# Performance work log

Measured on AMD Instinct MI355X. Metric: run time of the kernel, lower is better.

Reference implementation:

```python
import jax, jax.numpy as jnp
import numpy as np

B, T, I, H, L = 32768, 30, 4, 64, 32


def _lstm_layer(x, Wih, Whh, bih, bhh):
    """PyTorch-semantics single-layer LSTM, batch_first. Returns (outputs [B,T,H], h_T [B,H])."""
    # Precompute input contribution for all timesteps: [B, T, 4H]
    xg = jnp.einsum('bti,gi->btg', x, Wih) + bih + bhh
    Hh = Whh.shape[1]
    h0 = jnp.zeros((x.shape[0], Hh), x.dtype)

    def step(carry, xg_t):
        h, c = carry
        g = xg_t + h @ Whh.T  # [B, 4H]
        i, f, gg, o = jnp.split(g, 4, axis=-1)  # PyTorch gate order i,f,g,o
        c = jax.nn.sigmoid(f) * c + jax.nn.sigmoid(i) * jnp.tanh(gg)
        h = jax.nn.sigmoid(o) * jnp.tanh(c)
        return (h, c), h

    (hT, _), hs = jax.lax.scan(step, (h0, h0), jnp.swapaxes(xg, 0, 1))
    return jnp.swapaxes(hs, 0, 1), hT


def setup_inputs() -> dict:
    key = jax.random.key(0)
    ks = jax.random.split(key, 20)
    s = 0.1  # weight scale for numerical stability
    inp = {
        'x': jax.random.normal(ks[0], (B, T, I), jnp.float32),
        'enc1_Wih': s * jax.random.normal(ks[1], (4 * H, I), jnp.float32),
        'enc1_Whh': s * jax.random.normal(ks[2], (4 * H, H), jnp.float32),
        'enc1_bih': s * jax.random.normal(ks[3], (4 * H,), jnp.float32),
        'enc1_bhh': s * jax.random.normal(ks[4], (4 * H,), jnp.float32),
        'enc2_Wih': s * jax.random.normal(ks[5], (4 * L, H), jnp.float32),
        'enc2_Whh': s * jax.random.normal(ks[6], (4 * L, L), jnp.float32),
        'enc2_bih': s * jax.random.normal(ks[7], (4 * L,), jnp.float32),
        'enc2_bhh': s * jax.random.normal(ks[8], (4 * L,), jnp.float32),
        'dec1_Wih': s * jax.random.normal(ks[9], (4 * H, L), jnp.float32),
        'dec1_Whh': s * jax.random.normal(ks[10], (4 * H, H), jnp.float32),
        'dec1_bih': s * jax.random.normal(ks[11], (4 * H,), jnp.float32),
        'dec1_bhh': s * jax.random.normal(ks[12], (4 * H,), jnp.float32),
        'dec2_Wih': s * jax.random.normal(ks[13], (4 * I, H), jnp.float32),
        'dec2_Whh': s * jax.random.normal(ks[14], (4 * I, I), jnp.float32),
        'dec2_bih': s * jax.random.normal(ks[15], (4 * I,), jnp.float32),
        'dec2_bhh': s * jax.random.normal(ks[16], (4 * I,), jnp.float32),
    }
    return inp


def reference(x, enc1_Wih, enc1_Whh, enc1_bih, enc1_bhh,
              enc2_Wih, enc2_Whh, enc2_bih, enc2_bhh,
              dec1_Wih, dec1_Whh, dec1_bih, dec1_bhh,
              dec2_Wih, dec2_Whh, dec2_bih, dec2_bhh):
    seq_len = x.shape[1]
    out, _ = _lstm_layer(x, enc1_Wih, enc1_Whh, enc1_bih, enc1_bhh)
    out, h = _lstm_layer(out, enc2_Wih, enc2_Whh, enc2_bih, enc2_bhh)
    latent = jnp.repeat(h[:, None, :], seq_len, axis=1)  # [B, T, L]
    out, _ = _lstm_layer(latent, dec1_Wih, dec1_Whh, dec1_bih, dec1_bhh)
    out, _ = _lstm_layer(out, dec2_Wih, dec2_Whh, dec2_bih, dec2_bhh)
    return out
```

## Files before the change

### kernel.cpp

```cpp
#include <hip/hip_runtime.h>
#include <stdint.h>


typedef unsigned short u16;
typedef unsigned int u32;
typedef __attribute__((ext_vector_type(8))) short bf16x8;
typedef __attribute__((ext_vector_type(4))) float f32x4;
typedef __attribute__((ext_vector_type(4))) u32 u32x4;
typedef __attribute__((ext_vector_type(2))) u32 u32x2;

#define BATCH 32768
#define TT 30
#define IN 4
#define WAVES 8
#define BLOCKT (WAVES * 64)
#define MB 16
#define BPB (WAVES * MB)

#define LOG2E 1.4426950408889634f
#define LOG2E2 2.8853900817779268f

#define O_WHH1 0
#define O_W1C  8192
#define O_WIH2 9216
#define O_WHH2 13312
#define O_WHH3 0
#define O_WIH3 8192
#define O_WIH4 12288
#define O_W4HHF 12800
#define O_B1F 15360
#define O_B2F 15616
#define O_B3F 15744
#define O_B4F 16000
#define O_BUFS 16016
#define PBUF 1088
#define SMEM_WORDS (O_BUFS + WAVES * PBUF)
#define SMEM_BYTES (SMEM_WORDS * 4)

#define WB() __builtin_amdgcn_wave_barrier()
#define MFMA(a, b, c) __builtin_amdgcn_mfma_f32_16x16x32_bf16((a), (b), (c), 0, 0, 0)

__device__ __forceinline__ u16 f2bf(float f) {
    u32 u = __float_as_uint(f);
    u += 0x7fffu + ((u >> 16) & 1u);
    return (u16)(u >> 16);
}
__device__ __forceinline__ float bf2f(u16 v) { return __uint_as_float(((u32)v) << 16); }

__device__ __forceinline__ u32 cvtpk2(float a, float b) {
    u32 d;
    asm("v_cvt_pk_bf16_f32 %0, %1, %2" : "=v"(d) : "v"(a), "v"(b));
    return d;
}

__device__ __forceinline__ float unitH(float yi, float yf, float yg, float yo, float& c) {
    const float ei = __builtin_amdgcn_exp2f(-yi);
    const float ef = __builtin_amdgcn_exp2f(-yf);
    const float eg = __builtin_amdgcn_exp2f(yg);
    const float eo = __builtin_amdgcn_exp2f(-yo);
    const float Z = (1.f + ei) * (1.f + eg);
    const float X = 1.f + ef;
    const float num = fmaf(eg - 1.f, X, c * Z);
    c = num * __builtin_amdgcn_rcpf(X * Z);
    const float ec = __builtin_amdgcn_exp2f(c * LOG2E2);
    return (ec - 1.f) * __builtin_amdgcn_rcpf((1.f + eo) * (1.f + ec));
}

template <int KT, int GS>
__device__ __forceinline__ void stageBh(u16* hi, const float* src, int N, int tid) {
    const int K = KT * 32;
    const int total = N * K;
    for (int idx = tid; idx < total; idx += BLOCKT) {
        const int j = idx & 7;
        const int l = (idx >> 3) & 63;
        const int pr = idx >> 9;
        const int kt = pr & (KT - 1);
        const int nt = pr / KT;
        const int n = (nt << 4) | (l & 15);
        const int k = (kt << 5) + ((l >> 4) << 3) + j;
        const float s = (((n >> GS) & 3) == 2) ? LOG2E2 : LOG2E;
        hi[idx] = f2bf(src[n * K + k] * s);
    }
}

__global__ __launch_bounds__(BLOCKT)
__attribute__((amdgpu_waves_per_eu(2)))
void lstm_ae(
    const float* __restrict__ x,
    const float* __restrict__ w1ih, const float* __restrict__ w1hh,
    const float* __restrict__ b1i, const float* __restrict__ b1h,
    const float* __restrict__ w2ih, const float* __restrict__ w2hh,
    const float* __restrict__ b2i, const float* __restrict__ b2h,
    const float* __restrict__ w3ih, const float* __restrict__ w3hh,
    const float* __restrict__ b3i, const float* __restrict__ b3h,
    const float* __restrict__ w4ih, const float* __restrict__ w4hh,
    const float* __restrict__ b4i, const float* __restrict__ b4h,
    float* __restrict__ out) {
    extern __shared__ float smem[];
    float* W = smem;

    const int tid = threadIdx.x;
    const int wave = tid >> 6, lane = tid & 63;
    const int col = lane & 15, quad = lane >> 4;

    float* pb = smem + O_BUFS + wave * PBUF;
    u16* h1b = (u16*)pb;
    u16* h2b = (u16*)(pb + 512);
    float* gbuf = pb + 768;
    float* bufH4 = pb + 1024;

    const int b0w = blockIdx.x * BPB + wave * MB;
    const int hbase = (col << 3) + ((quad & 1) << 2) + ((quad >> 1) << 7);

    stageBh<2, 6>((u16*)(W + O_WHH1), w1hh, 256, tid);
    stageBh<2, 5>((u16*)(W + O_WIH2), w2ih, 128, tid);
    stageBh<1, 5>((u16*)(W + O_WHH2), w2hh, 128, tid);
    {
        u16* C = (u16*)(W + O_W1C);
        for (int idx = tid; idx < 2048; idx += BLOCKT) {
            const int n = idx >> 3, j = idx & 7;
            const float sc = ((n >> 6) == 2) ? LOG2E2 : LOG2E;
            const float w = w1ih[n * 4 + (j & 3)] * sc;
            C[idx] = (j < 4) ? f2bf(w) : f2bf(w - bf2f(f2bf(w)));
        }
    }
    float* b1f = W + O_B1F;
    float* b2f = W + O_B2F;
    float* b3f = W + O_B3F;
    float* b4f = W + O_B4F;
    for (int i = tid; i < 256; i += BLOCKT)
        b1f[i] = (b1i[i] + b1h[i]) * (((i >> 6) == 2) ? LOG2E2 : LOG2E);
    for (int i = tid; i < 128; i += BLOCKT)
        b2f[i] = (b2i[i] + b2h[i]) * (((i >> 5) == 2) ? LOG2E2 : LOG2E);
    for (int i = tid; i < 256; i += BLOCKT)
        b3f[i] = (b3i[i] + b3h[i]) * (((i >> 6) == 2) ? LOG2E2 : LOG2E);
    for (int i = tid; i < 16; i += BLOCKT)
        b4f[i] = (b4i[i] + b4h[i]) * (((i >> 2) == 2) ? LOG2E2 : LOG2E);
    {
        u32* z = (u32*)pb;
        for (int i = lane; i < 768; i += 64) z[i] = 0u;
    }
    __syncthreads();

    const u16* Whh1hi = (const u16*)(W + O_WHH1);
    const u16* Wih2hi = (const u16*)(W + O_WIH2);
    const u16* Whh2hi = (const u16*)(W + O_WHH2);
    const u16* W1cL = (const u16*)(W + O_W1C) + (col << 3) + ((quad == 1) ? 4 : 0);

    float c1[4][4];
    float c2[2][4];
#pragma unroll
    for (int q = 0; q < 4; ++q)
#pragma unroll
        for (int r = 0; r < 4; ++r) c1[q][r] = 0.f;
#pragma unroll
    for (int q = 0; q < 2; ++q)
#pragma unroll
        for (int r = 0; r < 4; ++r) c2[q][r] = 0.f;

    float4 xcur = *reinterpret_cast<const float4*>(x + ((size_t)(b0w + col) * TT + 0) * IN);

    for (int s = 0; s < TT; ++s) {
        const u32 hi01 = cvtpk2(xcur.x, xcur.y);
        const u32 hi23 = cvtpk2(xcur.z, xcur.w);
        const float r0 = xcur.x - __uint_as_float(hi01 << 16);
        const float r1 = xcur.y - __uint_as_float(hi01 & 0xffff0000u);
        const float r2 = xcur.z - __uint_as_float(hi23 << 16);
        const float r3 = xcur.w - __uint_as_float(hi23 & 0xffff0000u);
        const u32 lo01 = cvtpk2(r0, r1);
        const u32 lo23 = cvtpk2(r2, r3);
        u32x4 xv;
        xv.x = (quad <= 1) ? hi01 : 0u;
        xv.y = (quad <= 1) ? hi23 : 0u;
        xv.z = (quad == 0) ? lo01 : 0u;
        xv.w = (quad == 0) ? lo23 : 0u;
        const bf16x8 a1x = __builtin_bit_cast(bf16x8, xv);
        {
            const int tn = (s + 1 < TT) ? s + 1 : s;
            xcur = *reinterpret_cast<const float4*>(x + ((size_t)(b0w + col) * TT + tn) * IN);
        }
        const bf16x8 a1h0 = *reinterpret_cast<const bf16x8*>(h1b + lane * 8);
        const bf16x8 a1h1 = *reinterpret_cast<const bf16x8*>(h1b + (64 + lane) * 8);
#pragma unroll
        for (int q = 0; q < 4; ++q) {
            f32x4 acc[4];
#pragma unroll
            for (int i = 0; i < 4; ++i) {
                const int nt = i * 4 + q;
                const u32x2 wp = *reinterpret_cast<const u32x2*>(W1cL + nt * 128);
                u32x4 afu;
                afu.x = wp.x; afu.y = wp.y; afu.z = wp.x; afu.w = wp.y;
                const bf16x8 af = __builtin_bit_cast(bf16x8, afu);
                const bf16x8 bh0 = *reinterpret_cast<const bf16x8*>(Whh1hi + ((nt * 2 + 0) * 64 + lane) * 8);
                const bf16x8 bh1 = *reinterpret_cast<const bf16x8*>(Whh1hi + ((nt * 2 + 1) * 64 + lane) * 8);
                f32x4 a = *reinterpret_cast<const f32x4*>(b1f + nt * 16 + (quad << 2));
                a = MFMA(af, a1x, a);
                a = MFMA(bh0, a1h0, a);
                a = MFMA(bh1, a1h1, a);
                acc[i] = a;
            }
            const float h0 = unitH(acc[0][0], acc[1][0], acc[2][0], acc[3][0], c1[q][0]);
            const float h1 = unitH(acc[0][1], acc[1][1], acc[2][1], acc[3][1], c1[q][1]);
            const float h2 = unitH(acc[0][2], acc[1][2], acc[2][2], acc[3][2], c1[q][2]);
            const float h3 = unitH(acc[0][3], acc[1][3], acc[2][3], acc[3][3], c1[q][3]);
            u32x2 wv;
            wv.x = cvtpk2(h0, h1);
            wv.y = cvtpk2(h2, h3);
            *reinterpret_cast<u32x2*>(h1b + hbase + ((q >> 1) << 9) + ((q & 1) << 8)) = wv;
        }
        WB();
        const bf16x8 e1h0 = *reinterpret_cast<const bf16x8*>(h1b + lane * 8);
        const bf16x8 e1h1 = *reinterpret_cast<const bf16x8*>(h1b + (64 + lane) * 8);
        const bf16x8 a2h = *reinterpret_cast<const bf16x8*>(h2b + lane * 8);
        f32x4 acc2[8];
#pragma unroll
        for (int nt = 0; nt < 8; ++nt) {
            const bf16x8 bh0 = *reinterpret_cast<const bf16x8*>(Wih2hi + ((nt * 2 + 0) * 64 + lane) * 8);
            const bf16x8 bh1 = *reinterpret_cast<const bf16x8*>(Wih2hi + ((nt * 2 + 1) * 64 + lane) * 8);
            const bf16x8 ch = *reinterpret_cast<const bf16x8*>(Whh2hi + (nt * 64 + lane) * 8);
            f32x4 a = *reinterpret_cast<const f32x4*>(b2f + nt * 16 + (quad << 2));
            a = MFMA(bh0, e1h0, a);
            a = MFMA(bh1, e1h1, a);
            a = MFMA(ch, a2h, a);
            acc2[nt] = a;
        }
        WB();
#pragma unroll
        for (int q = 0; q < 2; ++q) {
            const float h0 = unitH(acc2[q][0], acc2[2 + q][0], acc2[4 + q][0], acc2[6 + q][0], c2[q][0]);
            const float h1 = unitH(acc2[q][1], acc2[2 + q][1], acc2[4 + q][1], acc2[6 + q][1], c2[q][1]);
            const float h2 = unitH(acc2[q][2], acc2[2 + q][2], acc2[4 + q][2], acc2[6 + q][2], c2[q][2]);
            const float h3 = unitH(acc2[q][3], acc2[2 + q][3], acc2[4 + q][3], acc2[6 + q][3], c2[q][3]);
            u32x2 wv;
            wv.x = cvtpk2(h0, h1);
            wv.y = cvtpk2(h2, h3);
            *reinterpret_cast<u32x2*>(h2b + hbase + (q << 8)) = wv;
        }
        WB();
    }

    __syncthreads();
    stageBh<2, 6>((u16*)(W + O_WHH3), w3hh, 256, tid);
    stageBh<1, 6>((u16*)(W + O_WIH3), w3ih, 256, tid);
    stageBh<2, 2>((u16*)(W + O_WIH4), w4ih, 16, tid);
    for (int i = tid; i < 64; i += BLOCKT)
        W[O_W4HHF + i] = w4hh[i] * ((((i >> 4) & 3) == 2) ? LOG2E2 : LOG2E);

    const bf16x8 aLh = *reinterpret_cast<const bf16x8*>(h2b + lane * 8);
    {
        u32* z = (u32*)pb;
        for (int i = lane; i < 512; i += 64) z[i] = 0u;
        bufH4[lane] = 0.f;
    }
    float c3[4][4];
#pragma unroll
    for (int q = 0; q < 4; ++q)
#pragma unroll
        for (int r = 0; r < 4; ++r) c3[q][r] = 0.f;
    float c4 = 0.f;
    const f32x4 bias4v = *reinterpret_cast<const f32x4*>(b4f + (quad << 2));
    const int u4 = lane & 3, mb = lane >> 2;
    __syncthreads();

    const u16* Whh3hi = (const u16*)(W + O_WHH3);
    const u16* Wih3hi = (const u16*)(W + O_WIH3);
    const u16* Wih4hi = (const u16*)(W + O_WIH4);
    const float* W4hhF = W + O_W4HHF;

    for (int s = 0; s < TT; ++s) {
        const bf16x8 a3h0 = *reinterpret_cast<const bf16x8*>(h1b + lane * 8);
        const bf16x8 a3h1 = *reinterpret_cast<const bf16x8*>(h1b + (64 + lane) * 8);
#pragma unroll
        for (int q = 0; q < 4; ++q) {
            f32x4 acc[4];
#pragma unroll
            for (int i = 0; i < 4; ++i) {
                const int nt = i * 4 + q;
                const bf16x8 bL = *reinterpret_cast<const bf16x8*>(Wih3hi + (nt * 64 + lane) * 8);
                const bf16x8 bh0 = *reinterpret_cast<const bf16x8*>(Whh3hi + ((nt * 2 + 0) * 64 + lane) * 8);
                const bf16x8 bh1 = *reinterpret_cast<const bf16x8*>(Whh3hi + ((nt * 2 + 1) * 64 + lane) * 8);
                f32x4 a = *reinterpret_cast<const f32x4*>(b3f + nt * 16 + (quad << 2));
                a = MFMA(bL, aLh, a);
                a = MFMA(bh0, a3h0, a);
                a = MFMA(bh1, a3h1, a);
                acc[i] = a;
            }
            const float h0 = unitH(acc[0][0], acc[1][0], acc[2][0], acc[3][0], c3[q][0]);
            const float h1 = unitH(acc[0][1], acc[1][1], acc[2][1], acc[3][1], c3[q][1]);
            const float h2 = unitH(acc[0][2], acc[1][2], acc[2][2], acc[3][2], c3[q][2]);
            const float h3 = unitH(acc[0][3], acc[1][3], acc[2][3], acc[3][3], c3[q][3]);
            u32x2 wv;
            wv.x = cvtpk2(h0, h1);
            wv.y = cvtpk2(h2, h3);
            *reinterpret_cast<u32x2*>(h1b + hbase + ((q >> 1) << 9) + ((q & 1) << 8)) = wv;
        }
        WB();
        const bf16x8 d3h0 = *reinterpret_cast<const bf16x8*>(h1b + lane * 8);
        const bf16x8 d3h1 = *reinterpret_cast<const bf16x8*>(h1b + (64 + lane) * 8);
        f32x4 acc4 = bias4v;
        {
            const float4 hv = *reinterpret_cast<const float4*>(bufH4 + (col << 2));
#pragma unroll
            for (int r = 0; r < 4; ++r) {
                const float4 w4 = *reinterpret_cast<const float4*>(W4hhF + ((quad * 4 + r) << 2));
                float sa = acc4[r];
                sa = fmaf(w4.x, hv.x, sa);
                sa = fmaf(w4.y, hv.y, sa);
                sa = fmaf(w4.z, hv.z, sa);
                sa = fmaf(w4.w, hv.w, sa);
                acc4[r] = sa;
            }
        }
        {
            const bf16x8 bh0 = *reinterpret_cast<const bf16x8*>(Wih4hi + (0 * 64 + lane) * 8);
            const bf16x8 bh1 = *reinterpret_cast<const bf16x8*>(Wih4hi + (1 * 64 + lane) * 8);
            acc4 = MFMA(bh0, d3h0, acc4);
            acc4 = MFMA(bh1, d3h1, acc4);
        }
        WB();
        *reinterpret_cast<f32x4*>(gbuf + (col << 4) + (quad << 2)) = acc4;
        WB();
        {
            const float yi = gbuf[mb * 16 + u4];
            const float yf = gbuf[mb * 16 + 4 + u4];
            const float yg = gbuf[mb * 16 + 8 + u4];
            const float yo = gbuf[mb * 16 + 12 + u4];
            const float h = unitH(yi, yf, yg, yo, c4);
            out[((size_t)(b0w + mb) * TT + s) * IN + u4] = h;
            bufH4[mb * 4 + u4] = h;
        }
        WB();
    }
}

extern "C" void kernel_launch(void* const* d_in, const int* in_sizes, int n_in,
                              void* d_out, int out_size, void* d_ws, size_t ws_size,
                              hipStream_t stream) {
    (void)in_sizes; (void)n_in; (void)d_ws; (void)ws_size; (void)out_size;
    hipFuncSetAttribute(reinterpret_cast<const void*>(lstm_ae),
                        hipFuncAttributeMaxDynamicSharedMemorySize, SMEM_BYTES);
    const float* xi = (const float*)d_in[0];
    const float* w1ih = (const float*)d_in[1];
    const float* w1hh = (const float*)d_in[2];
    const float* b1i = (const float*)d_in[3];
    const float* b1h = (const float*)d_in[4];
    const float* w2ih = (const float*)d_in[5];
    const float* w2hh = (const float*)d_in[6];
    const float* b2i = (const float*)d_in[7];
    const float* b2h = (const float*)d_in[8];
    const float* w3ih = (const float*)d_in[9];
    const float* w3hh = (const float*)d_in[10];
    const float* b3i = (const float*)d_in[11];
    const float* b3h = (const float*)d_in[12];
    const float* w4ih = (const float*)d_in[13];
    const float* w4hh = (const float*)d_in[14];
    const float* b4i = (const float*)d_in[15];
    const float* b4h = (const float*)d_in[16];
    float* out = (float*)d_out;

    lstm_ae<<<dim3(BATCH / BPB), dim3(BLOCKT), SMEM_BYTES, stream>>>(
        xi, w1ih, w1hh, b1i, b1h, w2ih, w2hh, b2i, b2h,
        w3ih, w3hh, b3i, b3h, w4ih, w4hh, b4i, b4h, out);
}
```

Baseline: 311.3 us.

## Split LSTM layers across wave roles in clusters with 32x32 MFMA tiles

Restructures the kernel so each block has 4 clusters of 3 waves working on 32 batch rows. Two waves per cluster compute the first layer's gates while the third runs the next layer one timestep behind, giving a software-pipelined wavefront across layers. The MFMA tiles move from 16x16x32 to 32x32x16, and the layer-1 input bias is folded into the input MFMA operand. This trades per-wave wave barriers for block-wide __syncthreads each step and makes the work imbalanced between roles.

```diff
diff --git a/kernel.cpp b/kernel.cpp
--- a/kernel.cpp
+++ b/kernel.cpp
@@ -6,39 +6,41 @@
 typedef unsigned int u32;
 typedef __attribute__((ext_vector_type(8))) short bf16x8;
 typedef __attribute__((ext_vector_type(4))) float f32x4;
+typedef __attribute__((ext_vector_type(16))) float f32x16;
 typedef __attribute__((ext_vector_type(4))) u32 u32x4;
 typedef __attribute__((ext_vector_type(2))) u32 u32x2;
 
 #define BATCH 32768
 #define TT 30
 #define IN 4
-#define WAVES 8
+#define WAVES 12
 #define BLOCKT (WAVES * 64)
-#define MB 16
-#define BPB (WAVES * MB)
+#define MBC 32
+#define NCL 4
+#define BPB (NCL * MBC)
 
 #define LOG2E 1.4426950408889634f
 #define LOG2E2 2.8853900817779268f
 
 #define O_WHH1 0
-#define O_W1C  8192
-#define O_WIH2 9216
-#define O_WHH2 13312
+#define O_FOLD 8192
+#define O_WIH2 10240
+#define O_WHH2 14336
 #define O_WHH3 0
 #define O_WIH3 8192
 #define O_WIH4 12288
 #define O_W4HHF 12800
-#define O_B1F 15360
-#define O_B2F 15616
-#define O_B3F 15744
-#define O_B4F 16000
-#define O_BUFS 16016
-#define PBUF 1088
-#define SMEM_WORDS (O_BUFS + WAVES * PBUF)
+#define O_B2F 16384
+#define O_B3F 16512
+#define O_B4F 16768
+#define O_BUFS 16784
+#define PBUF 1664
+#define SMEM_WORDS (O_BUFS + NCL * PBUF)
 #define SMEM_BYTES (SMEM_WORDS * 4)
 
 #define WB() __builtin_amdgcn_wave_barrier()
-#define MFMA(a, b, c) __builtin_amdgcn_mfma_f32_16x16x32_bf16((a), (b), (c), 0, 0, 0)
+#define MFMA32(a, b, c) __builtin_amdgcn_mfma_f32_32x32x16_bf16((a), (b), (c), 0, 0, 0)
+#define MFMA16(a, b, c) __builtin_amdgcn_mfma_f32_16x16x32_bf16((a), (b), (c), 0, 0, 0)
 
 __device__ __forceinline__ u16 f2bf(float f) {
     u32 u = __float_as_uint(f);
@@ -66,8 +68,25 @@
     return (ec - 1.f) * __builtin_amdgcn_rcpf((1.f + eo) * (1.f + ec));
 }
 
+template <int KT16, int GS>
+__device__ __forceinline__ void stage32(u16* dst, const float* src, int N, int tid) {
+    const int K = KT16 * 16;
+    const int total = N * K;
+    for (int idx = tid; idx < total; idx += BLOCKT) {
+        const int j = idx & 7;
+        const int l = (idx >> 3) & 63;
+        const int pr = idx >> 9;
+        const int kt = pr % KT16;
+        const int nt = pr / KT16;
+        const int n = nt * 32 + (l & 31);
+        const int k = kt * 16 + ((l >> 5) << 3) + j;
+        const float s = (((n >> GS) & 3) == 2) ? LOG2E2 : LOG2E;
+        dst[idx] = f2bf(src[n * K + k] * s);
+    }
+}
+
 template <int KT, int GS>
-__device__ __forceinline__ void stageBh(u16* hi, const float* src, int N, int tid) {
+__device__ __forceinline__ void stage16(u16* dst, const float* src, int N, int tid) {
     const int K = KT * 32;
     const int total = N * K;
     for (int idx = tid; idx < total; idx += BLOCKT) {
@@ -79,12 +98,97 @@
         const int n = (nt << 4) | (l & 15);
         const int k = (kt << 5) + ((l >> 4) << 3) + j;
         const float s = (((n >> GS) & 3) == 2) ? LOG2E2 : LOG2E;
-        hi[idx] = f2bf(src[n * K + k] * s);
-    }
-}
+        dst[idx] = f2bf(src[n * K + k] * s);
+    }
+}
+
+#define LD8(P, IDX) (*reinterpret_cast<const bf16x8*>((P) + ((IDX) * 64 + lane) * 8))
+
+#define BINIT(DST, BP, RB)                                                               \
+    _Pragma("unroll") for (int p_ = 0; p_ < 4; ++p_) {                                   \
+        const f32x4 b_ = *reinterpret_cast<const f32x4*>((BP) + (RB) + p_ * 8 + 4 * hi); \
+        (DST)[4 * p_ + 0] = b_[0]; (DST)[4 * p_ + 1] = b_[1];                            \
+        (DST)[4 * p_ + 2] = b_[2]; (DST)[4 * p_ + 3] = b_[3];                            \
+    }
+
+#define CELL16(AI, AF, AG, AO, CST, IMG, BKT)                                                        \
+    _Pragma("unroll") for (int p_ = 0; p_ < 4; ++p_) {                                               \
+        const float h0_ = unitH((AI)[4*p_+0], (AF)[4*p_+0], (AG)[4*p_+0], (AO)[4*p_+0], (CST)[4*p_+0]); \
+        const float h1_ = unitH((AI)[4*p_+1], (AF)[4*p_+1], (AG)[4*p_+1], (AO)[4*p_+1], (CST)[4*p_+1]); \
+        const float h2_ = unitH((AI)[4*p_+2], (AF)[4*p_+2], (AG)[4*p_+2], (AO)[4*p_+2], (CST)[4*p_+2]); \
+        const float h3_ = unitH((AI)[4*p_+3], (AF)[4*p_+3], (AG)[4*p_+3], (AO)[4*p_+3], (CST)[4*p_+3]); \
+        u32x2 wv_;                                                                                   \
+        wv_.x = cvtpk2(h0_, h1_);                                                                    \
+        wv_.y = cvtpk2(h2_, h3_);                                                                    \
+        *reinterpret_cast<u32x2*>((IMG) + (((BKT) + (p_ >> 1)) * 64 + (p_ & 1) * 32 + c31) * 8 + 4 * hi) = wv_; \
+    }
+
+#define E1G(DST, G) {                                                  \
+        f32x16 a_ = MFMA32(foldr[G], xB, z16);                         \
+        a_ = MFMA32(LD8(Whh1p, (2 * (G) + role) * 4 + 0), h1B0, a_);   \
+        a_ = MFMA32(LD8(Whh1p, (2 * (G) + role) * 4 + 1), h1B1, a_);   \
+        a_ = MFMA32(LD8(Whh1p, (2 * (G) + role) * 4 + 2), h1B2, a_);   \
+        a_ = MFMA32(LD8(Whh1p, (2 * (G) + role) * 4 + 3), h1B3, a_);   \
+        DST = a_; }
+
+#define E2G(DST, G) {                                                  \
+        f32x16 a_; BINIT(a_, b2f, (G) * 32)                            \
+        a_ = MFMA32(LD8(Wih2p, (G) * 4 + 0), h1B0, a_);                \
+        a_ = MFMA32(LD8(Wih2p, (G) * 4 + 1), h1B1, a_);                \
+        a_ = MFMA32(LD8(Wih2p, (G) * 4 + 2), h1B2, a_);                \
+        a_ = MFMA32(LD8(Wih2p, (G) * 4 + 3), h1B3, a_);                \
+        a_ = MFMA32(LD8(Whh2p, (G) * 2 + 0), h2B0, a_);                \
+        a_ = MFMA32(LD8(Whh2p, (G) * 2 + 1), h2B1, a_);                \
+        DST = a_; }
+
+#define D1G(DST, G) {                                                  \
+        f32x16 a_; BINIT(a_, b3f, (2 * (G) + role) * 32)               \
+        a_ = MFMA32(LD8(Wih3p, (2 * (G) + role) * 2 + 0), latB0, a_);  \
+        a_ = MFMA32(LD8(Wih3p, (2 * (G) + role) * 2 + 1), latB1, a_);  \
+        a_ = MFMA32(LD8(Whh3p, (2 * (G) + role) * 4 + 0), h3B0, a_);   \
+        a_ = MFMA32(LD8(Whh3p, (2 * (G) + role) * 4 + 1), h3B1, a_);   \
+        a_ = MFMA32(LD8(Whh3p, (2 * (G) + role) * 4 + 2), h3B2, a_);   \
+        a_ = MFMA32(LD8(Whh3p, (2 * (G) + role) * 4 + 3), h3B3, a_);   \
+        DST = a_; }
+#define D1G0(DST, G) {                                                 \
+        f32x16 a_; BINIT(a_, b3f, (2 * (G) + role) * 32)               \
+        a_ = MFMA32(LD8(Wih3p, (2 * (G) + role) * 2 + 0), latB0, a_);  \
+        a_ = MFMA32(LD8(Wih3p, (2 * (G) + role) * 2 + 1), latB1, a_);  \
+        DST = a_; }
+
+#define D2ADDR(M, BH) ((((2 * (M) + (quad >> 1)) * 64) + (quad & 1) * 32 + (BH) * 16 + col16) * 8)
+
+#define DEC2BODY(T) {                                                                   \
+        f32x4 a0 = b4v, a1 = b4v;                                                       \
+        _Pragma("unroll") for (int r_ = 0; r_ < 4; ++r_) {                              \
+            float s0 = a0[r_], s1 = a1[r_];                                             \
+            s0 = fmaf(w4r[r_].x, hv0.x, s0); s0 = fmaf(w4r[r_].y, hv0.y, s0);           \
+            s0 = fmaf(w4r[r_].z, hv0.z, s0); s0 = fmaf(w4r[r_].w, hv0.w, s0);           \
+            s1 = fmaf(w4r[r_].x, hv1.x, s1); s1 = fmaf(w4r[r_].y, hv1.y, s1);           \
+            s1 = fmaf(w4r[r_].z, hv1.z, s1); s1 = fmaf(w4r[r_].w, hv1.w, s1);           \
+            a0[r_] = s0; a1[r_] = s1;                                                   \
+        }                                                                               \
+        a0 = MFMA16(w4a0, dB00, a0); a0 = MFMA16(w4a1, dB10, a0);                       \
+        a1 = MFMA16(w4a0, dB01, a1); a1 = MFMA16(w4a1, dB11, a1);                       \
+        WB();                                                                           \
+        *reinterpret_cast<f32x4*>(gbuf + col16 * 16 + quad * 4) = a0;                   \
+        *reinterpret_cast<f32x4*>(gbuf + (16 + col16) * 16 + quad * 4) = a1;            \
+        WB();                                                                           \
+        {                                                                               \
+            const int u4_ = lane & 3, mb_ = lane >> 2;                                  \
+            const float h0_ = unitH(gbuf[mb_ * 16 + u4_], gbuf[mb_ * 16 + 4 + u4_],     \
+                                    gbuf[mb_ * 16 + 8 + u4_], gbuf[mb_ * 16 + 12 + u4_], c4a); \
+            out[((size_t)(b0w + mb_) * TT + (T)) * IN + u4_] = h0_;                     \
+            bufH4[mb_ * 4 + u4_] = h0_;                                                 \
+            const int b1_ = 16 + mb_;                                                   \
+            const float h1_ = unitH(gbuf[b1_ * 16 + u4_], gbuf[b1_ * 16 + 4 + u4_],     \
+                                    gbuf[b1_ * 16 + 8 + u4_], gbuf[b1_ * 16 + 12 + u4_], c4b); \
+            out[((size_t)(b0w + b1_) * TT + (T)) * IN + u4_] = h1_;                     \
+            bufH4[b1_ * 4 + u4_] = h1_;                                                 \
+        }                                                                               \
+        WB(); }
 
 __global__ __launch_bounds__(BLOCKT)
-__attribute__((amdgpu_waves_per_eu(2)))
 void lstm_ae(
     const float* __restrict__ x,
     const float* __restrict__ w1ih, const float* __restrict__ w1hh,
@@ -101,235 +205,223 @@
 
     const int tid = threadIdx.x;
     const int wave = tid >> 6, lane = tid & 63;
-    const int col = lane & 15, quad = lane >> 4;
-
-    float* pb = smem + O_BUFS + wave * PBUF;
-    u16* h1b = (u16*)pb;
-    u16* h2b = (u16*)(pb + 512);
-    float* gbuf = pb + 768;
-    float* bufH4 = pb + 1024;
-
-    const int b0w = blockIdx.x * BPB + wave * MB;
-    const int hbase = (col << 3) + ((quad & 1) << 2) + ((quad >> 1) << 7);
-
-    stageBh<2, 6>((u16*)(W + O_WHH1), w1hh, 256, tid);
-    stageBh<2, 5>((u16*)(W + O_WIH2), w2ih, 128, tid);
-    stageBh<1, 5>((u16*)(W + O_WHH2), w2hh, 128, tid);
+    const int cl = wave / 3, role = wave % 3;
+    const int c31 = lane & 31, hi = lane >> 5;
+    const int col16 = lane & 15, quad = lane >> 4;
+
+    float* pb = smem + O_BUFS + cl * PBUF;
+    u16* h1img = (u16*)pb;
+    u16* h2img = (u16*)(pb + 1024);
+    float* gbuf = pb + 1024;
+    float* bufH4 = pb + 1536;
+
+    const int b0w = blockIdx.x * BPB + cl * MBC;
+
+    stage32<4, 6>((u16*)(W + O_WHH1), w1hh, 256, tid);
+    stage32<4, 5>((u16*)(W + O_WIH2), w2ih, 128, tid);
+    stage32<2, 5>((u16*)(W + O_WHH2), w2hh, 128, tid);
     {
-        u16* C = (u16*)(W + O_W1C);
-        for (int idx = tid; idx < 2048; idx += BLOCKT) {
-            const int n = idx >> 3, j = idx & 7;
-            const float sc = ((n >> 6) == 2) ? LOG2E2 : LOG2E;
-            const float w = w1ih[n * 4 + (j & 3)] * sc;
-            C[idx] = (j < 4) ? f2bf(w) : f2bf(w - bf2f(f2bf(w)));
+        u16* F = (u16*)(W + O_FOLD);
+        for (int idx = tid; idx < 4096; idx += BLOCKT) {
+            const int j = idx & 7;
+            const int l = (idx >> 3) & 63;
+            const int nt = idx >> 9;
+            const int m = nt * 32 + (l & 31);
+            const int hif = l >> 5;
+            const float sc = ((m >> 6) == 2) ? LOG2E2 : LOG2E;
+            u16 v = 0;
+            if (!hif) {
+                v = f2bf(w1ih[m * 4 + (j & 3)] * sc);
+            } else if (j < 4) {
+                const float w = w1ih[m * 4 + j] * sc;
+                v = f2bf(w - bf2f(f2bf(w)));
+            } else if (j == 4) {
+                v = f2bf((b1i[m] + b1h[m]) * sc);
+            } else if (j == 5) {
+                const float b = (b1i[m] + b1h[m]) * sc;
+                v = f2bf(b - bf2f(f2bf(b)));
+            }
+            F[idx] = v;
         }
     }
-    float* b1f = W + O_B1F;
     float* b2f = W + O_B2F;
     float* b3f = W + O_B3F;
     float* b4f = W + O_B4F;
-    for (int i = tid; i < 256; i += BLOCKT)
-        b1f[i] = (b1i[i] + b1h[i]) * (((i >> 6) == 2) ? LOG2E2 : LOG2E);
     for (int i = tid; i < 128; i += BLOCKT)
         b2f[i] = (b2i[i] + b2h[i]) * (((i >> 5) == 2) ? LOG2E2 : LOG2E);
     for (int i = tid; i < 256; i += BLOCKT)
         b3f[i] = (b3i[i] + b3h[i]) * (((i >> 6) == 2) ? LOG2E2 : LOG2E);
     for (int i = tid; i < 16; i += BLOCKT)
         b4f[i] = (b4i[i] + b4h[i]) * (((i >> 2) == 2) ? LOG2E2 : LOG2E);
-    {
-        u32* z = (u32*)pb;
-        for (int i = lane; i < 768; i += 64) z[i] = 0u;
+    if (role == 2) {
+        u32* z = (u32*)h2img;
+        for (int i = lane; i < 512; i += 64) z[i] = 0u;
     }
     __syncthreads();
 
-    const u16* Whh1hi = (const u16*)(W + O_WHH1);
-    const u16* Wih2hi = (const u16*)(W + O_WIH2);
-    const u16* Whh2hi = (const u16*)(W + O_WHH2);
-    const u16* W1cL = (const u16*)(W + O_W1C) + (col << 3) + ((quad == 1) ? 4 : 0);
-
-    float c1[4][4];
-    float c2[2][4];
+    const u16* Whh1p = (const u16*)(W + O_WHH1);
+    const u16* Wih2p = (const u16*)(W + O_WIH2);
+    const u16* Whh2p = (const u16*)(W + O_WHH2);
+    const u16* FOLDp = (const u16*)(W + O_FOLD);
+
+    const f32x16 z16 = {0.f, 0.f, 0.f, 0.f, 0.f, 0.f, 0.f, 0.f,
+                        0.f, 0.f, 0.f, 0.f, 0.f, 0.f, 0.f, 0.f};
+    float cst[16];
 #pragma unroll
-    for (int q = 0; q < 4; ++q)
+    for (int r = 0; r < 16; ++r) cst[r] = 0.f;
+
+    bf16x8 foldr[4] = {};
+    if (role < 2) {
 #pragma unroll
-        for (int r = 0; r < 4; ++r) c1[q][r] = 0.f;
-#pragma unroll
-    for (int q = 0; q < 2; ++q)
-#pragma unroll
-        for (int r = 0; r < 4; ++r) c2[q][r] = 0.f;
-
-    float4 xcur = *reinterpret_cast<const float4*>(x + ((size_t)(b0w + col) * TT + 0) * IN);
-
-    for (int s = 0; s < TT; ++s) {
-        const u32 hi01 = cvtpk2(xcur.x, xcur.y);
-        const u32 hi23 = cvtpk2(xcur.z, xcur.w);
-        const float r0 = xcur.x - __uint_as_float(hi01 << 16);
-        const float r1 = xcur.y - __uint_as_float(hi01 & 0xffff0000u);
-        const float r2 = xcur.z - __uint_as_float(hi23 << 16);
-        const float r3 = xcur.w - __uint_as_float(hi23 & 0xffff0000u);
-        const u32 lo01 = cvtpk2(r0, r1);
-        const u32 lo23 = cvtpk2(r2, r3);
-        u32x4 xv;
-        xv.x = (quad <= 1) ? hi01 : 0u;
-        xv.y = (quad <= 1) ? hi23 : 0u;
-        xv.z = (quad == 0) ? lo01 : 0u;
-        xv.w = (quad == 0) ? lo23 : 0u;
-        const bf16x8 a1x = __builtin_bit_cast(bf16x8, xv);
-        {
-            const int tn = (s + 1 < TT) ? s + 1 : s;
-            xcur = *reinterpret_cast<const float4*>(x + ((size_t)(b0w + col) * TT + tn) * IN);
+        for (int g = 0; g < 4; ++g) foldr[g] = LD8(FOLDp, 2 * g + role);
+    }
+
+    float4 xcur = {0.f, 0.f, 0.f, 0.f};
+    if (role < 2)
+        xcur = *reinterpret_cast<const float4*>(x + ((size_t)(b0w + c31) * TT + 0) * IN);
+
+    auto buildX = [&](const float4 xc) -> bf16x8 {
+        const u32 h01 = cvtpk2(xc.x, xc.y);
+        const u32 h23 = cvtpk2(xc.z, xc.w);
+        const float r0 = xc.x - __uint_as_float(h01 << 16);
+        const float r1 = xc.y - __uint_as_float(h01 & 0xffff0000u);
+        const float r2 = xc.z - __uint_as_float(h23 << 16);
+        const float r3 = xc.w - __uint_as_float(h23 & 0xffff0000u);
+        const u32 l01 = cvtpk2(r0, r1);
+        const u32 l23 = cvtpk2(r2, r3);
+        u32x4 v;
+        v.x = h01;
+        v.y = h23;
+        v.z = hi ? 0x3F803F80u : l01;
+        v.w = hi ? 0u : l23;
+        return __builtin_bit_cast(bf16x8, v);
+    };
+
+    if (role < 2) {
+        const bf16x8 xB = buildX(xcur);
+        xcur = *reinterpret_cast<const float4*>(x + ((size_t)(b0w + c31) * TT + 1) * IN);
+        f32x16 aI = MFMA32(foldr[0], xB, z16);
+        f32x16 aF = MFMA32(foldr[1], xB, z16);
+        f32x16 aG = MFMA32(foldr[2], xB, z16);
+        f32x16 aO = MFMA32(foldr[3], xB, z16);
+        CELL16(aI, aF, aG, aO, cst, h1img, 2 * role)
+    }
+    __syncthreads();
+
+    for (int t = 0; t < TT - 1; ++t) {
+        const bf16x8 h1B0 = *reinterpret_cast<const bf16x8*>(h1img + (0 * 64 + lane) * 8);
+        const bf16x8 h1B1 = *reinterpret_cast<const bf16x8*>(h1img + (1 * 64 + lane) * 8);
+        const bf16x8 h1B2 = *reinterpret_cast<const bf16x8*>(h1img + (2 * 64 + lane) * 8);
+        const bf16x8 h1B3 = *reinterpret_cast<const bf16x8*>(h1img + (3 * 64 + lane) * 8);
+        bf16x8 h2B0 = {}, h2B1 = {};
+        if (role == 2) {
+            h2B0 = *reinterpret_cast<const bf16x8*>(h2img + (0 * 64 + lane) * 8);
+            h2B1 = *reinterpret_cast<const bf16x8*>(h2img + (1 * 64 + lane) * 8);
         }
-        const bf16x8 a1h0 = *reinterpret_cast<const bf16x8*>(h1b + lane * 8);
-        const bf16x8 a1h1 = *reinterpret_cast<const bf16x8*>(h1b + (64 + lane) * 8);
-#pragma unroll
-        for (int q = 0; q < 4; ++q) {
-            f32x4 acc[4];
-#pragma unroll
-            for (int i = 0; i < 4; ++i) {
-                const int nt = i * 4 + q;
-                const u32x2 wp = *reinterpret_cast<const u32x2*>(W1cL + nt * 128);
-                u32x4 afu;
-                afu.x = wp.x; afu.y = wp.y; afu.z = wp.x; afu.w = wp.y;
-                const bf16x8 af = __builtin_bit_cast(bf16x8, afu);
-                const bf16x8 bh0 = *reinterpret_cast<const bf16x8*>(Whh1hi + ((nt * 2 + 0) * 64 + lane) * 8);
-                const bf16x8 bh1 = *reinterpret_cast<const bf16x8*>(Whh1hi + ((nt * 2 + 1) * 64 + lane) * 8);
-                f32x4 a = *reinterpret_cast<const f32x4*>(b1f + nt * 16 + (quad << 2));
-                a = MFMA(af, a1x, a);
-                a = MFMA(bh0, a1h0, a);
-                a = MFMA(bh1, a1h1, a);
-                acc[i] = a;
-            }
-            const float h0 = unitH(acc[0][0], acc[1][0], acc[2][0], acc[3][0], c1[q][0]);
-            const float h1 = unitH(acc[0][1], acc[1][1], acc[2][1], acc[3][1], c1[q][1]);
-            const float h2 = unitH(acc[0][2], acc[1][2], acc[2][2], acc[3][2], c1[q][2]);
-            const float h3 = unitH(acc[0][3], acc[1][3], acc[2][3], acc[3][3], c1[q][3]);
-            u32x2 wv;
-            wv.x = cvtpk2(h0, h1);
-            wv.y = cvtpk2(h2, h3);
-            *reinterpret_cast<u32x2*>(h1b + hbase + ((q >> 1) << 9) + ((q & 1) << 8)) = wv;
+        __syncthreads();
+        if (role == 2) {
+            f32x16 aI, aF, aG, aO;
+            E2G(aI, 0) E2G(aF, 1) E2G(aG, 2) E2G(aO, 3)
+            CELL16(aI, aF, aG, aO, cst, h2img, 0)
+        } else {
+            const bf16x8 xB = buildX(xcur);
+            const int tn = (t + 2 < TT) ? t + 2 : TT - 1;
+            xcur = *reinterpret_cast<const float4*>(x + ((size_t)(b0w + c31) * TT + tn) * IN);
+            f32x16 aI, aF, aG, aO;
+            E1G(aI, 0) E1G(aF, 1) E1G(aG, 2) E1G(aO, 3)
+            CELL16(aI, aF, aG, aO, cst, h1img, 2 * role)
         }
-        WB();
-        const bf16x8 e1h0 = *reinterpret_cast<const bf16x8*>(h1b + lane * 8);
-        const bf16x8 e1h1 = *reinterpret_cast<const bf16x8*>(h1b + (64 + lane) * 8);
-        const bf16x8 a2h = *reinterpret_cast<const bf16x8*>(h2b + lane * 8);
-        f32x4 acc2[8];
-#pragma unroll
-        for (int nt = 0; nt < 8; ++nt) {
-            const bf16x8 bh0 = *reinterpret_cast<const bf16x8*>(Wih2hi + ((nt * 2 + 0) * 64 + lane) * 8);
-            const bf16x8 bh1 = *reinterpret_cast<const bf16x8*>(Wih2hi + ((nt * 2 + 1) * 64 + lane) * 8);
-            const bf16x8 ch = *reinterpret_cast<const bf16x8*>(Whh2hi + (nt * 64 + lane) * 8);
-            f32x4 a = *reinterpret_cast<const f32x4*>(b2f + nt * 16 + (quad << 2));
-            a = MFMA(bh0, e1h0, a);
-            a = MFMA(bh1, e1h1, a);
-            a = MFMA(ch, a2h, a);
-            acc2[nt] = a;
-        }
-        WB();
-#pragma unroll
-        for (int q = 0; q < 2; ++q) {
-            const float h0 = unitH(acc2[q][0], acc2[2 + q][0], acc2[4 + q][0], acc2[6 + q][0], c2[q][0]);
-            const float h1 = unitH(acc2[q][1], acc2[2 + q][1], acc2[4 + q][1], acc2[6 + q][1], c2[q][1]);
-            const float h2 = unitH(acc2[q][2], acc2[2 + q][2], acc2[4 + q][2], acc2[6 + q][2], c2[q][2]);
-            const float h3 = unitH(acc2[q][3], acc2[2 + q][3], acc2[4 + q][3], acc2[6 + q][3], c2[q][3]);
-            u32x2 wv;
-            wv.x = cvtpk2(h0, h1);
-            wv.y = cvtpk2(h2, h3);
-            *reinterpret_cast<u32x2*>(h2b + hbase + (q << 8)) = wv;
-        }
-        WB();
-    }
-
+        __syncthreads();
+    }
+    if (role == 2) {
+        const bf16x8 h1B0 = *reinterpret_cast<const bf16x8*>(h1img + (0 * 64 + lane) * 8);
+        const bf16x8 h1B1 = *reinterpret_cast<const bf16x8*>(h1img + (1 * 64 + lane) * 8);
+        const bf16x8 h1B2 = *reinterpret_cast<const bf16x8*>(h1img + (2 * 64 + lane) * 8);
+        const bf16x8 h1B3 = *reinterpret_cast<const bf16x8*>(h1img + (3 * 64 + lane) * 8);
+        const bf16x8 h2B0 = *reinterpret_cast<const bf16x8*>(h2img + (0 * 64 + lane) * 8);
+        const bf16x8 h2B1 = *reinterpret_cast<const bf16x8*>(h2img + (1 * 64 + lane) * 8);
+        f32x16 aI, aF, aG, aO;
+        E2G(aI, 0) E2G(aF, 1) E2G(aG, 2) E2G(aO, 3)
+        CELL16(aI, aF, aG, aO, cst, h2img, 0)
+    }
     __syncthreads();
-    stageBh<2, 6>((u16*)(W + O_WHH3), w3hh, 256, tid);
-    stageBh<1, 6>((u16*)(W + O_WIH3), w3ih, 256, tid);
-    stageBh<2, 2>((u16*)(W + O_WIH4), w4ih, 16, tid);
+
+    stage32<4, 6>((u16*)(W + O_WHH3), w3hh, 256, tid);
+    stage32<2, 6>((u16*)(W + O_WIH3), w3ih, 256, tid);
+    stage16<2, 2>((u16*)(W + O_WIH4), w4ih, 16, tid);
     for (int i = tid; i < 64; i += BLOCKT)
         W[O_W4HHF + i] = w4hh[i] * ((((i >> 4) & 3) == 2) ? LOG2E2 : LOG2E);
 
-    const bf16x8 aLh = *reinterpret_cast<const bf16x8*>(h2b + lane * 8);
-    {
-        u32* z = (u32*)pb;
-        for (int i = lane; i < 512; i += 64) z[i] = 0u;
-        bufH4[lane] = 0.f;
-    }
-    float c3[4][4];
+    float c4a = 0.f, c4b = 0.f;
+    bf16x8 latB0 = {}, latB1 = {};
+    if (role < 2) {
+        latB0 = *reinterpret_cast<const bf16x8*>(h2img + (0 * 64 + lane) * 8);
+        latB1 = *reinterpret_cast<const bf16x8*>(h2img + (1 * 64 + lane) * 8);
+    } else {
+        for (int i = lane; i < 128; i += 64) bufH4[i] = 0.f;
+    }
 #pragma unroll
-    for (int q = 0; q < 4; ++q)
+    for (int r = 0; r < 16; ++r) cst[r] = 0.f;
+    __syncthreads();
+
+    const u16* Whh3p = (const u16*)(W + O_WHH3);
+    const u16* Wih3p = (const u16*)(W + O_WIH3);
+    const u16* Wih4p = (const u16*)(W + O_WIH4);
+    const float* W4hhF = W + O_W4HHF;
+    bf16x8 w4a0 = {}, w4a1 = {};
+    f32x4 b4v = {0.f, 0.f, 0.f, 0.f};
+    float4 w4r[4] = {};
+    if (role == 2) {
+        w4a0 = LD8(Wih4p, 0);
+        w4a1 = LD8(Wih4p, 1);
+        b4v = *reinterpret_cast<const f32x4*>(b4f + quad * 4);
 #pragma unroll
-        for (int r = 0; r < 4; ++r) c3[q][r] = 0.f;
-    float c4 = 0.f;
-    const f32x4 bias4v = *reinterpret_cast<const f32x4*>(b4f + (quad << 2));
-    const int u4 = lane & 3, mb = lane >> 2;
+        for (int r = 0; r < 4; ++r)
+            w4r[r] = *reinterpret_cast<const float4*>(W4hhF + (quad * 4 + r) * 4);
+    }
+
+    if (role < 2) {
+        f32x16 aI, aF, aG, aO;
+        D1G0(aI, 0) D1G0(aF, 1) D1G0(aG, 2) D1G0(aO, 3)
+        CELL16(aI, aF, aG, aO, cst, h1img, 2 * role)
+    }
     __syncthreads();
 
-    const u16* Whh3hi = (const u16*)(W + O_WHH3);
-    const u16* Wih3hi = (const u16*)(W + O_WIH3);
-    const u16* Wih4hi = (const u16*)(W + O_WIH4);
-    const float* W4hhF = W + O_W4HHF;
-
-    for (int s = 0; s < TT; ++s) {
-        const bf16x8 a3h0 = *reinterpret_cast<const bf16x8*>(h1b + lane * 8);
-        const bf16x8 a3h1 = *reinterpret_cast<const bf16x8*>(h1b + (64 + lane) * 8);
-#pragma unroll
-        for (int q = 0; q < 4; ++q) {
-            f32x4 acc[4];
-#pragma unroll
-            for (int i = 0; i < 4; ++i) {
-                const int nt = i * 4 + q;
-                const bf16x8 bL = *reinterpret_cast<const bf16x8*>(Wih3hi + (nt * 64 + lane) * 8);
-                const bf16x8 bh0 = *reinterpret_cast<const bf16x8*>(Whh3hi + ((nt * 2 + 0) * 64 + lane) * 8);
-                const bf16x8 bh1 = *reinterpret_cast<const bf16x8*>(Whh3hi + ((nt * 2 + 1) * 64 + lane) * 8);
-                f32x4 a = *reinterpret_cast<const f32x4*>(b3f + nt * 16 + (quad << 2));
-                a = MFMA(bL, aLh, a);
-                a = MFMA(bh0, a3h0, a);
-                a = MFMA(bh1, a3h1, a);
-                acc[i] = a;
-            }
-            const float h0 = unitH(acc[0][0], acc[1][0], acc[2][0], acc[3][0], c3[q][0]);
-            const float h1 = unitH(acc[0][1], acc[1][1], acc[2][1], acc[3][1], c3[q][1]);
-            const float h2 = unitH(acc[0][2], acc[1][2], acc[2][2], acc[3][2], c3[q][2]);
-            const float h3 = unitH(acc[0][3], acc[1][3], acc[2][3], acc[3][3], c3[q][3]);
-            u32x2 wv;
-            wv.x = cvtpk2(h0, h1);
-            wv.y = cvtpk2(h2, h3);
-            *reinterpret_cast<u32x2*>(h1b + hbase + ((q >> 1) << 9) + ((q & 1) << 8)) = wv;
+    for (int t = 0; t < TT - 1; ++t) {
+        bf16x8 h3B0 = {}, h3B1 = {}, h3B2 = {}, h3B3 = {};
+        bf16x8 dB00 = {}, dB10 = {}, dB01 = {}, dB11 = {};
+        float4 hv0 = {0.f, 0.f, 0.f, 0.f}, hv1 = {0.f, 0.f, 0.f, 0.f};
+        if (role < 2) {
+            h3B0 = *reinterpret_cast<const bf16x8*>(h1img + (0 * 64 + lane) * 8);
+            h3B1 = *reinterpret_cast<const bf16x8*>(h1img + (1 * 64 + lane) * 8);
+            h3B2 = *reinterpret_cast<const bf16x8*>(h1img + (2 * 64 + lane) * 8);
+            h3B3 = *reinterpret_cast<const bf16x8*>(h1img + (3 * 64 + lane) * 8);
+        } else {
+            dB00 = *reinterpret_cast<const bf16x8*>(h1img + D2ADDR(0, 0));
+            dB10 = *reinterpret_cast<const bf16x8*>(h1img + D2ADDR(1, 0));
+            dB01 = *reinterpret_cast<const bf16x8*>(h1img + D2ADDR(0, 1));
+            dB11 = *reinterpret_cast<const bf16x8*>(h1img + D2ADDR(1, 1));
+            hv0 = *reinterpret_cast<const float4*>(bufH4 + col16 * 4);
+            hv1 = *reinterpret_cast<const float4*>(bufH4 + (16 + col16) * 4);
         }
-        WB();
-        const bf16x8 d3h0 = *reinterpret_cast<const bf16x8*>(h1b + lane * 8);
-        const bf16x8 d3h1 = *reinterpret_cast<const bf16x8*>(h1b + (64 + lane) * 8);
-        f32x4 acc4 = bias4v;
-        {
-            const float4 hv = *reinterpret_cast<const float4*>(bufH4 + (col << 2));
-#pragma unroll
-            for (int r = 0; r < 4; ++r) {
-                const float4 w4 = *reinterpret_cast<const float4*>(W4hhF + ((quad * 4 + r) << 2));
-                float sa = acc4[r];
-                sa = fmaf(w4.x, hv.x, sa);
-                sa = fmaf(w4.y, hv.y, sa);
-                sa = fmaf(w4.z, hv.z, sa);
-                sa = fmaf(w4.w, hv.w, sa);
-                acc4[r] = sa;
-            }
+        __syncthreads();
+        if (role == 2) {
+            DEC2BODY(t)
+        } else {
+            f32x16 aI, aF, aG, aO;
+            D1G(aI, 0) D1G(aF, 1) D1G(aG, 2) D1G(aO, 3)
+            CELL16(aI, aF, aG, aO, cst, h1img, 2 * role)
         }
-        {
-            const bf16x8 bh0 = *reinterpret_cast<const bf16x8*>(Wih4hi + (0 * 64 + lane) * 8);
-            const bf16x8 bh1 = *reinterpret_cast<const bf16x8*>(Wih4hi + (1 * 64 + lane) * 8);
-            acc4 = MFMA(bh0, d3h0, acc4);
-            acc4 = MFMA(bh1, d3h1, acc4);
-        }
-        WB();
-        *reinterpret_cast<f32x4*>(gbuf + (col << 4) + (quad << 2)) = acc4;
-        WB();
-        {
-            const float yi = gbuf[mb * 16 + u4];
-            const float yf = gbuf[mb * 16 + 4 + u4];
-            const float yg = gbuf[mb * 16 + 8 + u4];
-            const float yo = gbuf[mb * 16 + 12 + u4];
-            const float h = unitH(yi, yf, yg, yo, c4);
-            out[((size_t)(b0w + mb) * TT + s) * IN + u4] = h;
-            bufH4[mb * 4 + u4] = h;
-        }
-        WB();
+        __syncthreads();
+    }
+    if (role == 2) {
+        const bf16x8 dB00 = *reinterpret_cast<const bf16x8*>(h1img + D2ADDR(0, 0));
+        const bf16x8 dB10 = *reinterpret_cast<const bf16x8*>(h1img + D2ADDR(1, 0));
+        const bf16x8 dB01 = *reinterpret_cast<const bf16x8*>(h1img + D2ADDR(0, 1));
+        const bf16x8 dB11 = *reinterpret_cast<const bf16x8*>(h1img + D2ADDR(1, 1));
+        const float4 hv0 = *reinterpret_cast<const float4*>(bufH4 + col16 * 4);
+        const float4 hv1 = *reinterpret_cast<const float4*>(bufH4 + (16 + col16) * 4);
+        DEC2BODY(TT - 1)
     }
 }
 
```

New measurement: 286.1 us. 8.1% less time.
